# Performance work log

Hardware: AMD Instinct MI355X
Metric: run time of the kernel (lower is better)

The kernel has to match this reference:

```python
import jax, jax.numpy as jnp
import numpy as np

U, I, C, D, A, L, E = 40000, 40000, 5, 128, 64, 2, 1280000
N = U + I  # total graph nodes (users + items)
NEG_SLOPE = 0.01  # torch LeakyReLU default


def setup_inputs() -> dict:
    key = jax.random.key(0)
    ks = jax.random.split(key, 12)
    s = 0.05  # xavier-like scale
    return {
        "user_embed": jax.random.normal(ks[0], (U, C, D), jnp.float32) * s,
        "item_embed": jax.random.normal(ks[1], (I, C, D), jnp.float32) * s,
        "crit_embed": jax.random.normal(ks[2], (C, D), jnp.float32) * s,
        "gcn_weight": jax.random.normal(ks[3], (D, D), jnp.float32) * s,
        "gcn_layers": jax.random.normal(ks[4], (L, D, D), jnp.float32) * s,
        "crit_layers": jax.random.normal(ks[5], (L, D, D), jnp.float32) * s,
        "attn_p1": jax.random.normal(ks[6], (C, D, A), jnp.float32) * s,
        "attn_p2": jax.random.normal(ks[7], (C, A), jnp.float32) * s,
        "vals": jax.random.uniform(ks[8], (C, E), jnp.float32) / 16.0,
        "rows": jax.random.randint(ks[9], (C, E), 0, N, dtype=jnp.int32),
        "cols": jax.random.randint(ks[10], (C, E), 0, N, dtype=jnp.int32),
    }


def _forward(user_embed, item_embed, crit_embed, gcn_weight, gcn_layers,
             crit_layers, attn_p1, attn_p2, vals, rows, cols):
    ego = jnp.concatenate([user_embed, item_embed], axis=0)  # [N,C,D]
    bank = ego
    crit_hist = [crit_embed]  # list of [C,D], one per layer depth
    for l in range(L):
        crit_vec = crit_hist[l]  # [C,D]
        # per-criterion sparse adjacency matmul: A_c @ ego[:,c,:]
        feats = []
        for c in range(C):  # fixed small criterion count
            msg = vals[c][:, None] * jnp.take(ego[:, c, :], cols[c], axis=0)  # [E,D]
            feats.append(jax.ops.segment_sum(msg, rows[c], num_segments=N))
        gf = jnp.stack(feats, axis=1)                             # [N,C,D]
        gf = jnp.einsum('ncd,de->nce', gf, gcn_weight)            # dense GCN transform
        combined = gf * crit_vec[None, :, :]                      # criterion gating
        stacked = jax.nn.leaky_relu(
            jnp.einsum('ncd,de->nce', combined, gcn_layers[l]), NEG_SLOPE)  # [N,C,D]
        # tanh-attention aggregation, batched over the C output heads (k)
        h = jnp.tanh(jnp.einsum('ncd,kda->knca', stacked, attn_p1))  # [C,N,C,A]
        raw = jnp.einsum('knca,ka->knc', h, attn_p2)                 # [C,N,C]
        w = jax.nn.softmax(raw, axis=-1)                             # softmax over criteria
        ego = jnp.einsum('knc,ncd->nkd', w, stacked)                 # [N,C,D]
        bank = bank + ego
        crit_hist.append(crit_hist[l] @ crit_layers[l])  # [C,D]
    bank = bank / (L + 1)
    user_out = bank[:U]                                          # [U,C,D]
    item_out = jnp.concatenate(
        [bank[U:], jnp.zeros((1, C, D), bank.dtype)], axis=0)    # [I+1,C,D] dummy token
    crit_means = jnp.mean(jnp.stack(crit_hist, axis=0), axis=0)  # [C,D]
    return user_out, item_out, crit_means


def reference(user_embed, item_embed, crit_embed, gcn_weight, gcn_layers,
              crit_layers, attn_p1, attn_p2, vals, rows, cols):
    return _forward(user_embed, item_embed, crit_embed, gcn_weight, gcn_layers,
                    crit_layers, attn_p1, attn_p2, vals, rows, cols)
```

## Files before the change

### kernel.cpp

```cpp
#include <hip/hip_runtime.h>
#include <cstdint>
#include <cmath>

#define U_ 40000
#define I_ 40000
#define C_ 5
#define D_ 128
#define A_ 64
#define L_ 2
#define E_ 1280000
#define N_ (U_ + I_)
#define BINS_ (N_ * C_)
#define NEDGE_ (C_ * E_)
#define EPB_ 4096
#define NBRX_ ((NEDGE_ + EPB_ - 1) / EPB_)
#define ND1_ 1024
#define ND2_ 512

typedef __attribute__((ext_vector_type(8))) short short8;
typedef __attribute__((ext_vector_type(4))) short short4v;
typedef __attribute__((ext_vector_type(4))) float f32x4;

static __device__ __forceinline__ short f2bf(float f) {
    union { float f; uint32_t u; } x; x.f = f;
    uint32_t u = x.u;
    uint32_t r = (u + 0x7fffu + ((u >> 16) & 1u)) >> 16;
    return (short)r;
}

__global__ __launch_bounds__(256) void init_kernel(
    const float* __restrict__ user, const float* __restrict__ item,
    short* __restrict__ egob)
{
    size_t i = (size_t)blockIdx.x * 256 + threadIdx.x;
    const size_t total8 = (size_t)N_ * C_ * D_ / 8;
    const size_t user4  = (size_t)U_ * C_ * D_ / 4;
    if (i < total8) {
        size_t f4 = 2 * i;
        const float4* src = (f4 < user4) ? (const float4*)user
                                         : (const float4*)item - user4;
        float4 x0 = src[f4], x1 = src[f4 + 1];
        short8 p;
        p[0] = f2bf(x0.x); p[1] = f2bf(x0.y); p[2] = f2bf(x0.z); p[3] = f2bf(x0.w);
        p[4] = f2bf(x1.x); p[5] = f2bf(x1.y); p[6] = f2bf(x1.z); p[7] = f2bf(x1.w);
        ((short8*)egob)[i] = p;
    }
}

__global__ __launch_bounds__(128) void crit_kernel(
    const float* __restrict__ crit0, const float* __restrict__ clayers,
    float* __restrict__ crit1, float* __restrict__ crit2,
    float* __restrict__ crit_means, float* __restrict__ padrow)
{
    __shared__ float c0[C_ * D_], c1[C_ * D_], c2[C_ * D_];
    int t = threadIdx.x;
    for (int i = t; i < C_ * D_; i += 128) { c0[i] = crit0[i]; padrow[i] = 0.f; }
    __syncthreads();
    for (int c = 0; c < C_; ++c) {
        float acc = 0.f;
        for (int d = 0; d < D_; ++d) acc = fmaf(c0[c * D_ + d], clayers[d * D_ + t], acc);
        c1[c * D_ + t] = acc;
    }
    __syncthreads();
    for (int c = 0; c < C_; ++c) {
        float acc = 0.f;
        for (int d = 0; d < D_; ++d) acc = fmaf(c1[c * D_ + d], clayers[D_ * D_ + d * D_ + t], acc);
        c2[c * D_ + t] = acc;
    }
    __syncthreads();
    for (int i = t; i < C_ * D_; i += 128) {
        crit1[i] = c1[i];
        crit2[i] = c2[i];
        crit_means[i] = (c0[i] + c1[i] + c2[i]) * (1.0f / 3.0f);
    }
}

__global__ __launch_bounds__(256) void prepack_kernel(
    const float* __restrict__ W, const float* __restrict__ gl,
    short* __restrict__ Wf, short* __restrict__ Gf)
{
    int b = blockIdx.x;
    int m = b >> 3, t = b & 7;
    int q = threadIdx.x >> 6, l = threadIdx.x & 63;
    int g = l >> 4, c15 = l & 15;
    const float* src = (m == 0) ? W : gl + (size_t)(m - 1) * D_ * D_;
    short*       dst = (m == 0) ? Wf : Gf + (size_t)(m - 1) * D_ * D_;
    short8 v;
    #pragma unroll
    for (int j = 0; j < 8; ++j) {
        int k = q * 32 + g * 8 + j;
        int n = t * 16 + c15;
        v[j] = f2bf(src[k * D_ + n]);
    }
    *(short8*)(dst + (((t * 4 + q) * 64 + l) << 3)) = v;
}

__global__ __launch_bounds__(64) void prepack_p1_kernel(
    const float* __restrict__ p1, short* __restrict__ P1f)
{
    int t = blockIdx.x >> 2, q = blockIdx.x & 3;
    int lane = threadIdx.x;
    int g = lane >> 4, c15 = lane & 15;
    int k = t >> 2, a = (t & 3) * 16 + c15;
    short8 v;
    #pragma unroll
    for (int j = 0; j < 8; ++j) {
        int d = q * 32 + g * 8 + j;
        v[j] = f2bf(p1[((size_t)k * D_ + d) * A_ + a]);
    }
    *(short8*)(P1f + (((t * 4 + q) * 64 + lane) << 3)) = v;
}


__global__ __launch_bounds__(256) void p1_count_kernel(
    const int* __restrict__ rows, int* __restrict__ ghistT)
{
    __shared__ int h[ND1_];
    int b = blockIdx.x, tid = threadIdx.x;
    for (int i = tid; i < ND1_; i += 256) h[i] = 0;
    __syncthreads();
    int base = b * EPB_;
    for (int ch = 0; ch < EPB_ / 256; ++ch) {
        int eid = base + ch * 256 + tid;
        if (eid < NEDGE_) {
            int key = (eid / E_) * N_ + rows[eid];
            atomicAdd(&h[key & (ND1_ - 1)], 1);
        }
    }
    __syncthreads();
    for (int i = tid; i < ND1_; i += 256) ghistT[b * ND1_ + i] = h[i];
}

__global__ __launch_bounds__(256) void transpose_kernel(
    const int* __restrict__ src, int* __restrict__ dst, int R, int Cc)
{
    int i = blockIdx.x * 256 + threadIdx.x;
    if (i < R * Cc) { int r = i / Cc, c = i % Cc; dst[c * R + r] = src[i]; }
}

__global__ __launch_bounds__(256) void scanA_g(
    const int* __restrict__ src, int* __restrict__ dst,
    int* __restrict__ bsum, int n)
{
    __shared__ int ls[256];
    int b = blockIdx.x, t = threadIdx.x;
    int base = b * 1024 + t * 4;
    int v[4];
    #pragma unroll
    for (int i = 0; i < 4; ++i) v[i] = (base + i < n) ? src[base + i] : 0;
    int s = v[0] + v[1] + v[2] + v[3];
    ls[t] = s;
    __syncthreads();
    for (int off = 1; off < 256; off <<= 1) {
        int x = (t >= off) ? ls[t - off] : 0;
        __syncthreads();
        ls[t] += x;
        __syncthreads();
    }
    int excl = ls[t] - s;
    if (t == 255) bsum[b] = ls[255];
    #pragma unroll
    for (int i = 0; i < 4; ++i) {
        if (base + i < n) dst[base + i] = excl;
        excl += v[i];
    }
}

__global__ __launch_bounds__(256) void scanB_g(int* __restrict__ bsum, int nb)
{
    __shared__ int ls[256];
    int t = threadIdx.x;
    int v[8]; int s = 0;
    #pragma unroll
    for (int i = 0; i < 8; ++i) {
        int idx = t * 8 + i;
        v[i] = (idx < nb) ? bsum[idx] : 0;
        s += v[i];
    }
    ls[t] = s;
    __syncthreads();
    for (int off = 1; off < 256; off <<= 1) {
        int x = (t >= off) ? ls[t - off] : 0;
        __syncthreads();
        ls[t] += x;
        __syncthreads();
    }
    int excl = ls[t] - s;
    #pragma unroll
    for (int i = 0; i < 8; ++i) {
        int idx = t * 8 + i;
        if (idx < nb) bsum[idx] = excl;
        excl += v[i];
    }
}

__global__ __launch_bounds__(256) void scanC_g(
    int* __restrict__ dst, const int* __restrict__ bsum, int n)
{
    int b = blockIdx.x, t = threadIdx.x;
    int off = bsum[b];
    int base = b * 1024 + t * 4;
    #pragma unroll
    for (int i = 0; i < 4; ++i)
        if (base + i < n) dst[base + i] += off;
}

__global__ __launch_bounds__(256) void p1_place_kernel(
    const int* __restrict__ rows, const float* __restrict__ vals,
    const int* __restrict__ cols, const int* __restrict__ gbaseT,
    int* __restrict__ keyA, uint2* __restrict__ vcA)
{
    __shared__ int cur[ND1_];
    __shared__ int bst[ND1_];
    __shared__ int gb[ND1_];
    __shared__ int ts[256];
    __shared__ int sK[EPB_];
    __shared__ uint2 sV[EPB_];
    int b = blockIdx.x, tid = threadIdx.x;
    for (int i = tid; i < ND1_; i += 256) { cur[i] = 0; gb[i] = gbaseT[b * ND1_ + i]; }
    __syncthreads();
    int base = b * EPB_;
    for (int ch = 0; ch < EPB_ / 256; ++ch) {
        int eid = base + ch * 256 + tid;
        if (eid < NEDGE_) {
            int key = (eid / E_) * N_ + rows[eid];
            atomicAdd(&cur[key & (ND1_ - 1)], 1);
        }
    }
    __syncthreads();
    {
        int v[4]; int s = 0;
        #pragma unroll
        for (int i = 0; i < 4; ++i) { v[i] = cur[tid * 4 + i]; s += v[i]; }
        ts[tid] = s;
        __syncthreads();
        for (int off = 1; off < 256; off <<= 1) {
            int x = (tid >= off) ? ts[tid - off] : 0;
            __syncthreads();
            ts[tid] += x;
            __syncthreads();
        }
        int excl = ts[tid] - s;
        #pragma unroll
        for (int i = 0; i < 4; ++i) { bst[tid * 4 + i] = excl; excl += v[i]; }
        __syncthreads();
        #pragma unroll
        for (int i = 0; i < 4; ++i) cur[tid * 4 + i] = bst[tid * 4 + i];
    }
    __syncthreads();
    for (int ch = 0; ch < EPB_ / 256; ++ch) {
        int eid = base + ch * 256 + tid;
        if (eid < NEDGE_) {
            int key = (eid / E_) * N_ + rows[eid];
            int d = key & (ND1_ - 1);
            int p = atomicAdd(&cur[d], 1);
            sK[p] = key;
            union { float f; uint32_t u; } t; t.f = vals[eid];
            uint2 m; m.x = t.u; m.y = (uint32_t)cols[eid];
            sV[p] = m;
        }
    }
    __syncthreads();
    int M = NEDGE_ - base; if (M > EPB_) M = EPB_;
    for (int i = tid; i < M; i += 256) {
        int key = sK[i]; int d = key & (ND1_ - 1);
        int pos = gb[d] + (i - bst[d]);
        keyA[pos] = key; vcA[pos] = sV[i];
    }
}

__global__ __launch_bounds__(256) void p2_count_kernel(
    const int* __restrict__ keyA, int* __restrict__ ghistT)
{
    __shared__ int h[ND2_];
    int b = blockIdx.x, tid = threadIdx.x;
    for (int i = tid; i < ND2_; i += 256) h[i] = 0;
    __syncthreads();
    int base = b * EPB_;
    for (int ch = 0; ch < EPB_ / 256; ++ch) {
        int eid = base + ch * 256 + tid;
        if (eid < NEDGE_) atomicAdd(&h[keyA[eid] >> 10], 1);
    }
    __syncthreads();
    for (int i = tid; i < ND2_; i += 256) ghistT[b * ND2_ + i] = h[i];
}

__global__ __launch_bounds__(256) void p2_place_kernel(
    const int* __restrict__ keyA, const uint2* __restrict__ vcA,
    const int* __restrict__ gbaseT,
    int* __restrict__ keyB, uint2* __restrict__ vcB)
{
    __shared__ int cur[ND2_];
    __shared__ int bst[ND2_];
    __shared__ int gb[ND2_];
    __shared__ int wh[4 * ND2_];
    __shared__ int ts[256];
    __shared__ int sK[EPB_];
    __shared__ uint2 sV[EPB_];
    int b = blockIdx.x, tid = threadIdx.x;
    int lane = tid & 63, wv = tid >> 6;
    for (int i = tid; i < ND2_; i += 256) { cur[i] = 0; gb[i] = gbaseT[b * ND2_ + i]; }
    __syncthreads();
    int base = b * EPB_;
    for (int ch = 0; ch < EPB_ / 256; ++ch) {
        int eid = base + ch * 256 + tid;
        if (eid < NEDGE_) atomicAdd(&cur[keyA[eid] >> 10], 1);
    }
    __syncthreads();
    {
        int v0 = cur[tid * 2], v1 = cur[tid * 2 + 1];
        int s = v0 + v1;
        ts[tid] = s;
        __syncthreads();
        for (int off = 1; off < 256; off <<= 1) {
            int x = (tid >= off) ? ts[tid - off] : 0;
            __syncthreads();
            ts[tid] += x;
            __syncthreads();
        }
        int excl = ts[tid] - s;
        bst[tid * 2] = excl; bst[tid * 2 + 1] = excl + v0;
        __syncthreads();
        cur[tid * 2] = bst[tid * 2]; cur[tid * 2 + 1] = bst[tid * 2 + 1];
    }
    __syncthreads();
    for (int ch = 0; ch < EPB_ / 256; ++ch) {
        for (int i = tid; i < 4 * ND2_; i += 256) wh[i] = 0;
        __syncthreads();
        int eid = base + ch * 256 + tid;
        bool valid = eid < NEDGE_;
        int key = 0, d = 0; uint2 v = make_uint2(0u, 0u);
        if (valid) { key = keyA[eid]; v = vcA[eid]; d = key >> 10; }
        unsigned long long m = __ballot(valid ? 1 : 0);
        #pragma unroll
        for (int bit = 0; bit < 9; ++bit) {
            unsigned long long bb = __ballot((valid && ((d >> bit) & 1)) ? 1 : 0);
            m &= ((d >> bit) & 1) ? bb : ~bb;
        }
        unsigned long long ltm = ((unsigned long long)1 << lane) - 1;
        int rw = __popcll(m & ltm);
        int cnt = __popcll(m);
        if (valid && rw == 0) wh[wv * ND2_ + d] = cnt;
        __syncthreads();
        if (valid) {
            int off = 0;
            for (int w2 = 0; w2 < wv; ++w2) off += wh[w2 * ND2_ + d];
            int p = cur[d] + off + rw;
            sK[p] = key; sV[p] = v;
        }
        __syncthreads();
        for (int i = tid; i < ND2_; i += 256)
            cur[i] += wh[i] + wh[ND2_ + i] + wh[2 * ND2_ + i] + wh[3 * ND2_ + i];
        __syncthreads();
    }
    int M = NEDGE_ - base; if (M > EPB_) M = EPB_;
    for (int i = tid; i < M; i += 256) {
        int key = sK[i]; int d = key >> 10;
        int pos = gb[d] + (i - bst[d]);
        keyB[pos] = key; vcB[pos] = sV[i];
    }
}

__global__ __launch_bounds__(256) void boundary_kernel(
    const int* __restrict__ keyB, int* __restrict__ bin_start)
{
    int i = blockIdx.x * 256 + threadIdx.x;
    if (i >= NEDGE_) return;
    int k = keyB[i];
    if (i == 0) {
        for (int b = 0; b <= k; ++b) bin_start[b] = 0;
    } else {
        int kp = keyB[i - 1];
        for (int b = kp + 1; b <= k; ++b) bin_start[b] = i;
    }
    if (i == NEDGE_ - 1) {
        for (int b = k + 1; b <= BINS_; ++b) bin_start[b] = NEDGE_;
    }
}

__global__ __launch_bounds__(256) void gather_kernel(
    const uint4* __restrict__ eg128, const uint2* __restrict__ vc,
    const int* __restrict__ bin_start, uint4* __restrict__ gfb128)
{
    int w = (int)(((size_t)blockIdx.x * 256 + threadIdx.x) >> 6);
    int lane = threadIdx.x & 63;
    w = __builtin_amdgcn_readfirstlane(w);
    int bs = bin_start[w], be = bin_start[w + 1];
    int c = w / N_;
    int row = w - c * N_;
    int q4 = lane >> 4, l15 = lane & 15;
    float a0 = 0.f, a1 = 0.f, a2 = 0.f, a3 = 0.f;
    float a4 = 0.f, a5 = 0.f, a6 = 0.f, a7 = 0.f;

    union { uint32_t u; float f; } t;
    #define ACC8(mm, vv) \
        t.u = mm.x << 16;         a0 = fmaf(vv, t.f, a0); \
        t.u = mm.x & 0xffff0000u; a1 = fmaf(vv, t.f, a1); \
        t.u = mm.y << 16;         a2 = fmaf(vv, t.f, a2); \
        t.u = mm.y & 0xffff0000u; a3 = fmaf(vv, t.f, a3); \
        t.u = mm.z << 16;         a4 = fmaf(vv, t.f, a4); \
        t.u = mm.z & 0xffff0000u; a5 = fmaf(vv, t.f, a5); \
        t.u = mm.w << 16;         a6 = fmaf(vv, t.f, a6); \
        t.u = mm.w & 0xffff0000u; a7 = fmaf(vv, t.f, a7);

    int j = bs;
    for (; j + 16 <= be; j += 16) {
        uint2 eA = vc[j + q4];
        uint2 eB = vc[j + 4 + q4];
        uint2 eC = vc[j + 8 + q4];
        uint2 eD = vc[j + 12 + q4];
        uint4 mA = eg128[((size_t)(int)eA.y * C_ + c) * (D_ / 8) + l15];
        uint4 mB = eg128[((size_t)(int)eB.y * C_ + c) * (D_ / 8) + l15];
        uint4 mC = eg128[((size_t)(int)eC.y * C_ + c) * (D_ / 8) + l15];
        uint4 mD = eg128[((size_t)(int)eD.y * C_ + c) * (D_ / 8) + l15];
        union { uint32_t u; float f; } fv;
        fv.u = eA.x; float vA = fv.f;
        fv.u = eB.x; float vB = fv.f;
        fv.u = eC.x; float vC = fv.f;
        fv.u = eD.x; float vD = fv.f;
        ACC8(mA, vA) ACC8(mB, vB) ACC8(mC, vC) ACC8(mD, vD)
    }
    for (; j < be; j += 4) {
        int idx = j + q4;
        bool act = idx < be;
        uint2 e0 = vc[act ? idx : be - 1];
        union { uint32_t u; float f; } fv; fv.u = e0.x;
        float v0 = act ? fv.f : 0.f;
        uint4 m0 = eg128[((size_t)(int)e0.y * C_ + c) * (D_ / 8) + l15];
        ACC8(m0, v0)
    }
    #undef ACC8

    a0 += __shfl_xor(a0, 16); a1 += __shfl_xor(a1, 16);
    a2 += __shfl_xor(a2, 16); a3 += __shfl_xor(a3, 16);
    a4 += __shfl_xor(a4, 16); a5 += __shfl_xor(a5, 16);
    a6 += __shfl_xor(a6, 16); a7 += __shfl_xor(a7, 16);
    a0 += __shfl_xor(a0, 32); a1 += __shfl_xor(a1, 32);
    a2 += __shfl_xor(a2, 32); a3 += __shfl_xor(a3, 32);
    a4 += __shfl_xor(a4, 32); a5 += __shfl_xor(a5, 32);
    a6 += __shfl_xor(a6, 32); a7 += __shfl_xor(a7, 32);
    if (lane < 16) {
        uint4 o;
        o.x = (uint32_t)(uint16_t)f2bf(a0) | ((uint32_t)(uint16_t)f2bf(a1) << 16);
        o.y = (uint32_t)(uint16_t)f2bf(a2) | ((uint32_t)(uint16_t)f2bf(a3) << 16);
        o.z = (uint32_t)(uint16_t)f2bf(a4) | ((uint32_t)(uint16_t)f2bf(a5) << 16);
        o.w = (uint32_t)(uint16_t)f2bf(a6) | ((uint32_t)(uint16_t)f2bf(a7) << 16);
        gfb128[((size_t)row * C_ + c) * (D_ / 8) + l15] = o;
    }
}

__global__ __launch_bounds__(1024, 4) void rowgemm_mfma_kernel(
    const short* __restrict__ gfb, short* __restrict__ stkb,
    const short* __restrict__ Wf, const short* __restrict__ Gf,
    const float* __restrict__ critv)
{
    __shared__ short Wl[16384];
    __shared__ short Gl[16384];
    __shared__ short Zr[16][2048];

    for (int i = threadIdx.x; i < 2048; i += 1024) {
        ((short8*)Wl)[i] = ((const short8*)Wf)[i];
        ((short8*)Gl)[i] = ((const short8*)Gf)[i];
    }
    __syncthreads();

    int lane = threadIdx.x & 63, w = threadIdx.x >> 6;
    int g = lane >> 4, c15 = lane & 15;
    char* zw = (char*)&Zr[w][0];
    const int nrb = (N_ * C_ + 255) / 256;

    for (int rb = blockIdx.x; rb < nrb; rb += gridDim.x) {
        size_t r0 = (size_t)rb * 256 + (size_t)w * 16;
        if (r0 >= N_ * C_) continue;

        short8 af[4];
        #pragma unroll
        for (int q = 0; q < 4; ++q)
            af[q] = *(const short8*)(gfb + (r0 + c15) * D_ + q * 32 + g * 8);

        f32x4 acc[8];
        #pragma unroll
        for (int t = 0; t < 8; ++t) acc[t] = (f32x4){0.f, 0.f, 0.f, 0.f};
        {
            const short8* Wp = (const short8*)Wl;
            #pragma unroll
            for (int t = 0; t < 8; ++t)
                #pragma unroll
                for (int q = 0; q < 4; ++q)
                    acc[t] = __builtin_amdgcn_mfma_f32_16x16x32_bf16(
                        af[q], Wp[(t * 4 + q) * 64 + lane], acc[t], 0, 0, 0);
        }

        int rbase = (int)r0 + g * 4;
        #pragma unroll
        for (int t = 0; t < 8; ++t)
            #pragma unroll
            for (int r = 0; r < 4; ++r) {
                float cv = critv[((rbase + r) % C_) * D_ + t * 16 + c15];
                float z = acc[t][r] * cv;
                int zrow = g * 4 + r;
                int cb = 32 * t + 2 * c15;
                int off = zrow * 256 + (cb ^ ((zrow & 7) << 4));
                *(short*)(zw + off) = f2bf(z);
            }

        short8 az[4];
        #pragma unroll
        for (int q = 0; q < 4; ++q) {
            int cb0 = 64 * q + 16 * g;
            int off = c15 * 256 + (cb0 ^ ((c15 & 7) << 4));
            az[q] = *(const short8*)(zw + off);
        }

        f32x4 acc2[8];
        #pragma unroll
        for (int t = 0; t < 8; ++t) acc2[t] = (f32x4){0.f, 0.f, 0.f, 0.f};
        {
            const short8* Gp = (const short8*)Gl;
            #pragma unroll
            for (int t = 0; t < 8; ++t)
                #pragma unroll
                for (int q = 0; q < 4; ++q)
                    acc2[t] = __builtin_amdgcn_mfma_f32_16x16x32_bf16(
                        Gp[(t * 4 + q) * 64 + lane], az[q], acc2[t], 0, 0, 0);
        }

        short* srow = stkb + (r0 + c15) * D_;
        #pragma unroll
        for (int t = 0; t < 8; ++t) {
            float s0 = acc2[t][0], s1 = acc2[t][1], s2 = acc2[t][2], s3 = acc2[t][3];
            s0 = s0 > 0.f ? s0 : 0.01f * s0;
            s1 = s1 > 0.f ? s1 : 0.01f * s1;
            s2 = s2 > 0.f ? s2 : 0.01f * s2;
            s3 = s3 > 0.f ? s3 : 0.01f * s3;
            uint2 o;
            o.x = (uint32_t)(uint16_t)f2bf(s0) | ((uint32_t)(uint16_t)f2bf(s1) << 16);
            o.y = (uint32_t)(uint16_t)f2bf(s2) | ((uint32_t)(uint16_t)f2bf(s3) << 16);
            *(uint2*)(srow + t * 16 + g * 4) = o;
        }
    }
}

__global__ __launch_bounds__(256, 3) void attn_mfma_kernel(
    const short* __restrict__ stkb, const short* __restrict__ P1f,
    const float* __restrict__ p2, const float* __restrict__ user,
    const float* __restrict__ item, short* __restrict__ egob,
    float* __restrict__ bank, int last)
{
    __shared__ float rawl[80 * C_];
    __shared__ float wl[80 * C_];

    int tid = threadIdx.x;
    int lane = tid & 63, w = tid >> 6;
    int g = lane >> 4, c15 = lane & 15;
    int klo = (5 * w) >> 2;

    short8 Bf[5][4];
    float p2v[5];
    #pragma unroll
    for (int i = 0; i < 5; ++i) {
        int t = 5 * w + i;
        #pragma unroll
        for (int q = 0; q < 4; ++q)
            Bf[i][q] = ((const short8*)P1f)[(t * 4 + q) * 64 + lane];
        p2v[i] = p2[(t >> 2) * A_ + (t & 3) * 16 + c15];
    }

    float4*       bank4 = (float4*)bank;
    const float4* user4 = (const float4*)user;
    const float4* item4 = (const float4*)item;

    for (int grp = blockIdx.x; grp < N_ / 16; grp += gridDim.x) {
        size_t n0 = (size_t)grp * 16;
        for (int i = tid; i < 80 * C_; i += 256) rawl[i] = 0.f;
        __syncthreads();

        for (int rt = 0; rt < 5; ++rt) {
            short8 af[4];
            #pragma unroll
            for (int q = 0; q < 4; ++q)
                af[q] = *(const short8*)(stkb + (n0 * 5 + rt * 16 + c15) * D_ + q * 32 + g * 8);

            f32x4 acc[5];
            #pragma unroll
            for (int i = 0; i < 5; ++i) acc[i] = (f32x4){0.f, 0.f, 0.f, 0.f};
            #pragma unroll
            for (int i = 0; i < 5; ++i)
                #pragma unroll
                for (int q = 0; q < 4; ++q)
                    acc[i] = __builtin_amdgcn_mfma_f32_16x16x32_bf16(
                        af[q], Bf[i][q], acc[i], 0, 0, 0);

            float2 ps[4];
            #pragma unroll
            for (int r = 0; r < 4; ++r) ps[r] = make_float2(0.f, 0.f);
            #pragma unroll
            for (int i = 0; i < 5; ++i) {
                int t = 5 * w + i;
                bool lo = (t >> 2) == klo;
                #pragma unroll
                for (int r = 0; r < 4; ++r) {
                    float x = acc[i][r];
                    float e = __expf(2.f * x);
                    float th = 1.f - 2.f * __builtin_amdgcn_rcpf(e + 1.f);
                    float con = th * p2v[i];
                    if (lo) ps[r].x += con; else ps[r].y += con;
                }
            }
            #pragma unroll
            for (int r = 0; r < 4; ++r) {
                #pragma unroll
                for (int m = 1; m < 16; m <<= 1) {
                    ps[r].x += __shfl_xor(ps[r].x, m);
                    ps[r].y += __shfl_xor(ps[r].y, m);
                }
                if (c15 == 0) {
                    int row = rt * 16 + g * 4 + r;
                    atomicAdd(&rawl[row * C_ + klo], ps[r].x);
                    atomicAdd(&rawl[row * C_ + klo + 1], ps[r].y);
                }
            }
        }
        __syncthreads();

        if (tid < 80) {
            int nl = tid / C_, k = tid % C_;
            float rv[C_];
            #pragma unroll
            for (int c = 0; c < C_; ++c) rv[c] = rawl[(nl * C_ + c) * C_ + k];
            float m = rv[0];
            #pragma unroll
            for (int c = 1; c < C_; ++c) m = fmaxf(m, rv[c]);
            float s = 0.f;
            #pragma unroll
            for (int c = 0; c < C_; ++c) { rv[c] = __expf(rv[c] - m); s += rv[c]; }
            float inv = __builtin_amdgcn_rcpf(s);
            #pragma unroll
            for (int c = 0; c < C_; ++c) wl[tid * C_ + c] = rv[c] * inv;
        }
        __syncthreads();

        #pragma unroll
        for (int ii = 0; ii < 5; ++ii) {
            int idx = tid + 256 * ii;
            int f8 = idx & 15;
            int nl = (idx >> 4) & 15, k = idx >> 8;
            float e[8] = {0.f, 0.f, 0.f, 0.f, 0.f, 0.f, 0.f, 0.f};
            #pragma unroll
            for (int c = 0; c < C_; ++c) {
                float wv = wl[(nl * C_ + k) * C_ + c];
                uint4 sv = ((const uint4*)(stkb + ((n0 + nl) * C_ + c) * D_))[f8];
                union { uint32_t u; float f; } t;
                t.u = sv.x << 16;         e[0] = fmaf(wv, t.f, e[0]);
                t.u = sv.x & 0xffff0000u; e[1] = fmaf(wv, t.f, e[1]);
                t.u = sv.y << 16;         e[2] = fmaf(wv, t.f, e[2]);
                t.u = sv.y & 0xffff0000u; e[3] = fmaf(wv, t.f, e[3]);
                t.u = sv.z << 16;         e[4] = fmaf(wv, t.f, e[4]);
                t.u = sv.z & 0xffff0000u; e[5] = fmaf(wv, t.f, e[5]);
                t.u = sv.w << 16;         e[6] = fmaf(wv, t.f, e[6]);
                t.u = sv.w & 0xffff0000u; e[7] = fmaf(wv, t.f, e[7]);
            }
            size_t n = n0 + nl;
            size_t go = ((n * 5 + k) * 16 + f8) * 8;
            if (!last) {
                short8 pk;
                #pragma unroll
                for (int x = 0; x < 8; ++x) pk[x] = f2bf(e[x]);
                *(short8*)(egob + go) = pk;
            } else {
                uint4 e0 = *(const uint4*)(egob + go);
                size_t bo = (n * 5 + k) * 32 + f8 * 2;
                float4 b0 = (n < U_) ? user4[((size_t)n * C_ + k) * 32 + f8 * 2]
                                     : item4[((size_t)(n - U_) * C_ + k) * 32 + f8 * 2];
                float4 b1 = (n < U_) ? user4[((size_t)n * C_ + k) * 32 + f8 * 2 + 1]
                                     : item4[((size_t)(n - U_) * C_ + k) * 32 + f8 * 2 + 1];
                union { uint32_t u; float f; } t;
                t.u = e0.x << 16;         b0.x += t.f + e[0];
                t.u = e0.x & 0xffff0000u; b0.y += t.f + e[1];
                t.u = e0.y << 16;         b0.z += t.f + e[2];
                t.u = e0.y & 0xffff0000u; b0.w += t.f + e[3];
                t.u = e0.z << 16;         b1.x += t.f + e[4];
                t.u = e0.z & 0xffff0000u; b1.y += t.f + e[5];
                t.u = e0.w << 16;         b1.z += t.f + e[6];
                t.u = e0.w & 0xffff0000u; b1.w += t.f + e[7];
                b0.x *= (1.f / 3.f); b0.y *= (1.f / 3.f);
                b0.z *= (1.f / 3.f); b0.w *= (1.f / 3.f);
                b1.x *= (1.f / 3.f); b1.y *= (1.f / 3.f);
                b1.z *= (1.f / 3.f); b1.w *= (1.f / 3.f);
                bank4[bo] = b0;
                bank4[bo + 1] = b1;
            }
        }
    }
}

extern "C" void kernel_launch(void* const* d_in, const int* in_sizes, int n_in,
                              void* d_out, int out_size, void* d_ws, size_t ws_size,
                              hipStream_t stream) {
    const float* user  = (const float*)d_in[0];
    const float* item  = (const float*)d_in[1];
    const float* crit0 = (const float*)d_in[2];
    const float* W     = (const float*)d_in[3];
    const float* gl    = (const float*)d_in[4];
    const float* cl    = (const float*)d_in[5];
    const float* p1    = (const float*)d_in[6];
    const float* p2    = (const float*)d_in[7];
    const float* vals  = (const float*)d_in[8];
    const int*   rows  = (const int*)d_in[9];
    const int*   cols  = (const int*)d_in[10];

    float* out  = (float*)d_out;
    float* bank = out;
    float* padrow = out + (size_t)N_ * C_ * D_;
    float* crit_means = out + (size_t)(N_ + 1) * C_ * D_;

    const size_t NCD = (size_t)N_ * C_ * D_;
    short* egob  = (short*)d_ws;
    short* gfb   = egob + NCD;
    short* stkb  = gfb + NCD;
    float* crit1 = (float*)(stkb + NCD);
    float* crit2 = crit1 + C_ * D_;
    short* Wf    = (short*)(crit2 + C_ * D_);
    short* Gf    = Wf + (size_t)D_ * D_;
    short* P1f   = Gf + 2 * (size_t)D_ * D_;
    int* bin_start = (int*)(P1f + (size_t)D_ * C_ * A_);
    int* keyB      = bin_start + BINS_ + 2;
    uint2* vcB     = (uint2*)(keyB + NEDGE_);
    int* ghist     = (int*)(vcB + NEDGE_);
    int* ghistT    = ghist + (size_t)ND1_ * NBRX_;
    int* bsum      = ghistT + (size_t)ND1_ * NBRX_;
    uint2* vcA = (uint2*)stkb;
    int*  keyA = (int*)((char*)stkb + (size_t)NEDGE_ * 8);

    init_kernel<<<(int)((NCD / 8 + 255) / 256), 256, 0, stream>>>(user, item, egob);
    crit_kernel<<<1, 128, 0, stream>>>(crit0, cl, crit1, crit2, crit_means, padrow);
    prepack_kernel<<<24, 256, 0, stream>>>(W, gl, Wf, Gf);
    prepack_p1_kernel<<<80, 64, 0, stream>>>(p1, P1f);

    const int n1 = ND1_ * NBRX_, n2 = ND2_ * NBRX_;
    p1_count_kernel<<<NBRX_, 256, 0, stream>>>(rows, ghistT);
    transpose_kernel<<<(n1 + 255) / 256, 256, 0, stream>>>(ghistT, ghist, NBRX_, ND1_);
    scanA_g<<<(n1 + 1023) / 1024, 256, 0, stream>>>(ghist, ghist, bsum, n1);
    scanB_g<<<1, 256, 0, stream>>>(bsum, (n1 + 1023) / 1024);
    scanC_g<<<(n1 + 1023) / 1024, 256, 0, stream>>>(ghist, bsum, n1);
    transpose_kernel<<<(n1 + 255) / 256, 256, 0, stream>>>(ghist, ghistT, ND1_, NBRX_);
    p1_place_kernel<<<NBRX_, 256, 0, stream>>>(rows, vals, cols, ghistT, keyA, vcA);

    p2_count_kernel<<<NBRX_, 256, 0, stream>>>(keyA, ghistT);
    transpose_kernel<<<(n2 + 255) / 256, 256, 0, stream>>>(ghistT, ghist, NBRX_, ND2_);
    scanA_g<<<(n2 + 1023) / 1024, 256, 0, stream>>>(ghist, ghist, bsum, n2);
    scanB_g<<<1, 256, 0, stream>>>(bsum, (n2 + 1023) / 1024);
    scanC_g<<<(n2 + 1023) / 1024, 256, 0, stream>>>(ghist, bsum, n2);
    transpose_kernel<<<(n2 + 255) / 256, 256, 0, stream>>>(ghist, ghistT, ND2_, NBRX_);
    p2_place_kernel<<<NBRX_, 256, 0, stream>>>(keyA, vcA, ghistT, keyB, vcB);

    boundary_kernel<<<(NEDGE_ + 255) / 256, 256, 0, stream>>>(keyB, bin_start);

    for (int l = 0; l < L_; ++l) {
        gather_kernel<<<BINS_ / 4, 256, 0, stream>>>(
            (const uint4*)egob, vcB, bin_start, (uint4*)gfb);
        rowgemm_mfma_kernel<<<256, 1024, 0, stream>>>(
            gfb, stkb, Wf, Gf + (size_t)l * D_ * D_, l == 0 ? crit0 : crit1);
        attn_mfma_kernel<<<768, 256, 0, stream>>>(
            stkb, P1f, p2, user, item, egob, bank, l == L_ - 1 ? 1 : 0);
    }
}
```

Measured before the change: 1.335 ms.

## Reuse saved per-block histograms in place kernels and shuffle-broadcast edge metadata in gather

The count kernels now also save each block's per-bucket histogram to a separate buffer. The place kernels read those counts instead of re-reading the keys and redoing shared-memory atomics, which removes a full pass over the edge data and some barriers. The gather kernel now loads up to 64 edge (value, column) pairs cooperatively, one per lane, and broadcasts them with shuffles, instead of having each 4-lane group reload them from global memory. The trade-off is an extra histogram buffer placed after bsum, which relies on the workspace being large enough, plus extra shuffle instructions in the gather inner loop.

```diff
diff --git a/kernel.cpp b/kernel.cpp
--- a/kernel.cpp
+++ b/kernel.cpp
@@ -113,7 +113,8 @@
 
 
 __global__ __launch_bounds__(256) void p1_count_kernel(
-    const int* __restrict__ rows, int* __restrict__ ghistT)
+    const int* __restrict__ rows, int* __restrict__ ghistT,
+    int* __restrict__ gcntT)
 {
     __shared__ int h[ND1_];
     int b = blockIdx.x, tid = threadIdx.x;
@@ -128,7 +129,10 @@
         }
     }
     __syncthreads();
-    for (int i = tid; i < ND1_; i += 256) ghistT[b * ND1_ + i] = h[i];
+    for (int i = tid; i < ND1_; i += 256) {
+        ghistT[b * ND1_ + i] = h[i];
+        gcntT[b * ND1_ + i] = h[i];
+    }
 }
 
 __global__ __launch_bounds__(256) void transpose_kernel(
@@ -208,6 +212,7 @@
 __global__ __launch_bounds__(256) void p1_place_kernel(
     const int* __restrict__ rows, const float* __restrict__ vals,
     const int* __restrict__ cols, const int* __restrict__ gbaseT,
+    const int* __restrict__ gcntT,
     int* __restrict__ keyA, uint2* __restrict__ vcA)
 {
     __shared__ int cur[ND1_];
@@ -217,21 +222,11 @@
     __shared__ int sK[EPB_];
     __shared__ uint2 sV[EPB_];
     int b = blockIdx.x, tid = threadIdx.x;
-    for (int i = tid; i < ND1_; i += 256) { cur[i] = 0; gb[i] = gbaseT[b * ND1_ + i]; }
-    __syncthreads();
-    int base = b * EPB_;
-    for (int ch = 0; ch < EPB_ / 256; ++ch) {
-        int eid = base + ch * 256 + tid;
-        if (eid < NEDGE_) {
-            int key = (eid / E_) * N_ + rows[eid];
-            atomicAdd(&cur[key & (ND1_ - 1)], 1);
-        }
-    }
-    __syncthreads();
+    for (int i = tid; i < ND1_; i += 256) gb[i] = gbaseT[b * ND1_ + i];
     {
         int v[4]; int s = 0;
         #pragma unroll
-        for (int i = 0; i < 4; ++i) { v[i] = cur[tid * 4 + i]; s += v[i]; }
+        for (int i = 0; i < 4; ++i) { v[i] = gcntT[b * ND1_ + tid * 4 + i]; s += v[i]; }
         ts[tid] = s;
         __syncthreads();
         for (int off = 1; off < 256; off <<= 1) {
@@ -242,12 +237,10 @@
         }
         int excl = ts[tid] - s;
         #pragma unroll
-        for (int i = 0; i < 4; ++i) { bst[tid * 4 + i] = excl; excl += v[i]; }
-        __syncthreads();
-        #pragma unroll
-        for (int i = 0; i < 4; ++i) cur[tid * 4 + i] = bst[tid * 4 + i];
-    }
-    __syncthreads();
+        for (int i = 0; i < 4; ++i) { bst[tid * 4 + i] = excl; cur[tid * 4 + i] = excl; excl += v[i]; }
+    }
+    __syncthreads();
+    int base = b * EPB_;
     for (int ch = 0; ch < EPB_ / 256; ++ch) {
         int eid = base + ch * 256 + tid;
         if (eid < NEDGE_) {
@@ -270,7 +263,8 @@
 }
 
 __global__ __launch_bounds__(256) void p2_count_kernel(
-    const int* __restrict__ keyA, int* __restrict__ ghistT)
+    const int* __restrict__ keyA, int* __restrict__ ghistT,
+    int* __restrict__ gcntT)
 {
     __shared__ int h[ND2_];
     int b = blockIdx.x, tid = threadIdx.x;
@@ -282,12 +276,15 @@
         if (eid < NEDGE_) atomicAdd(&h[keyA[eid] >> 10], 1);
     }
     __syncthreads();
-    for (int i = tid; i < ND2_; i += 256) ghistT[b * ND2_ + i] = h[i];
+    for (int i = tid; i < ND2_; i += 256) {
+        ghistT[b * ND2_ + i] = h[i];
+        gcntT[b * ND2_ + i] = h[i];
+    }
 }
 
 __global__ __launch_bounds__(256) void p2_place_kernel(
     const int* __restrict__ keyA, const uint2* __restrict__ vcA,
-    const int* __restrict__ gbaseT,
+    const int* __restrict__ gbaseT, const int* __restrict__ gcntT,
     int* __restrict__ keyB, uint2* __restrict__ vcB)
 {
     __shared__ int cur[ND2_];
@@ -299,16 +296,10 @@
     __shared__ uint2 sV[EPB_];
     int b = blockIdx.x, tid = threadIdx.x;
     int lane = tid & 63, wv = tid >> 6;
-    for (int i = tid; i < ND2_; i += 256) { cur[i] = 0; gb[i] = gbaseT[b * ND2_ + i]; }
-    __syncthreads();
-    int base = b * EPB_;
-    for (int ch = 0; ch < EPB_ / 256; ++ch) {
-        int eid = base + ch * 256 + tid;
-        if (eid < NEDGE_) atomicAdd(&cur[keyA[eid] >> 10], 1);
-    }
-    __syncthreads();
+    for (int i = tid; i < ND2_; i += 256) gb[i] = gbaseT[b * ND2_ + i];
+    for (int i = tid; i < 4 * ND2_; i += 256) wh[i] = 0;
     {
-        int v0 = cur[tid * 2], v1 = cur[tid * 2 + 1];
+        int v0 = gcntT[b * ND2_ + tid * 2], v1 = gcntT[b * ND2_ + tid * 2 + 1];
         int s = v0 + v1;
         ts[tid] = s;
         __syncthreads();
@@ -320,13 +311,11 @@
         }
         int excl = ts[tid] - s;
         bst[tid * 2] = excl; bst[tid * 2 + 1] = excl + v0;
-        __syncthreads();
-        cur[tid * 2] = bst[tid * 2]; cur[tid * 2 + 1] = bst[tid * 2 + 1];
-    }
-    __syncthreads();
+        cur[tid * 2] = excl; cur[tid * 2 + 1] = excl + v0;
+    }
+    __syncthreads();
+    int base = b * EPB_;
     for (int ch = 0; ch < EPB_ / 256; ++ch) {
-        for (int i = tid; i < 4 * ND2_; i += 256) wh[i] = 0;
-        __syncthreads();
         int eid = base + ch * 256 + tid;
         bool valid = eid < NEDGE_;
         int key = 0, d = 0; uint2 v = make_uint2(0u, 0u);
@@ -349,8 +338,10 @@
             sK[p] = key; sV[p] = v;
         }
         __syncthreads();
-        for (int i = tid; i < ND2_; i += 256)
+        for (int i = tid; i < ND2_; i += 256) {
             cur[i] += wh[i] + wh[ND2_ + i] + wh[2 * ND2_ + i] + wh[3 * ND2_ + i];
+            wh[i] = 0; wh[ND2_ + i] = 0; wh[2 * ND2_ + i] = 0; wh[3 * ND2_ + i] = 0;
+        }
         __syncthreads();
     }
     int M = NEDGE_ - base; if (M > EPB_) M = EPB_;
@@ -392,45 +383,45 @@
     float a0 = 0.f, a1 = 0.f, a2 = 0.f, a3 = 0.f;
     float a4 = 0.f, a5 = 0.f, a6 = 0.f, a7 = 0.f;
 
-    union { uint32_t u; float f; } t;
-    #define ACC8(mm, vv) \
-        t.u = mm.x << 16;         a0 = fmaf(vv, t.f, a0); \
-        t.u = mm.x & 0xffff0000u; a1 = fmaf(vv, t.f, a1); \
-        t.u = mm.y << 16;         a2 = fmaf(vv, t.f, a2); \
-        t.u = mm.y & 0xffff0000u; a3 = fmaf(vv, t.f, a3); \
-        t.u = mm.z << 16;         a4 = fmaf(vv, t.f, a4); \
-        t.u = mm.z & 0xffff0000u; a5 = fmaf(vv, t.f, a5); \
-        t.u = mm.w << 16;         a6 = fmaf(vv, t.f, a6); \
-        t.u = mm.w & 0xffff0000u; a7 = fmaf(vv, t.f, a7);
-
-    int j = bs;
-    for (; j + 16 <= be; j += 16) {
-        uint2 eA = vc[j + q4];
-        uint2 eB = vc[j + 4 + q4];
-        uint2 eC = vc[j + 8 + q4];
-        uint2 eD = vc[j + 12 + q4];
-        uint4 mA = eg128[((size_t)(int)eA.y * C_ + c) * (D_ / 8) + l15];
-        uint4 mB = eg128[((size_t)(int)eB.y * C_ + c) * (D_ / 8) + l15];
-        uint4 mC = eg128[((size_t)(int)eC.y * C_ + c) * (D_ / 8) + l15];
-        uint4 mD = eg128[((size_t)(int)eD.y * C_ + c) * (D_ / 8) + l15];
-        union { uint32_t u; float f; } fv;
-        fv.u = eA.x; float vA = fv.f;
-        fv.u = eB.x; float vB = fv.f;
-        fv.u = eC.x; float vC = fv.f;
-        fv.u = eD.x; float vD = fv.f;
-        ACC8(mA, vA) ACC8(mB, vB) ACC8(mC, vC) ACC8(mD, vD)
-    }
-    for (; j < be; j += 4) {
-        int idx = j + q4;
-        bool act = idx < be;
-        uint2 e0 = vc[act ? idx : be - 1];
-        union { uint32_t u; float f; } fv; fv.u = e0.x;
-        float v0 = act ? fv.f : 0.f;
-        uint4 m0 = eg128[((size_t)(int)e0.y * C_ + c) * (D_ / 8) + l15];
-        ACC8(m0, v0)
-    }
-    #undef ACC8
-
+    for (int base = bs; base < be; base += 64) {
+        int cnt = be - base; if (cnt > 64) cnt = 64;
+        float v = 0.f; int s = 0;
+        if (lane < cnt) {
+            uint2 m = vc[base + lane];
+            union { uint32_t u; float f; } t; t.u = m.x;
+            v = t.f; s = (int)m.y;
+        }
+        int j = 0;
+        for (; j + 16 <= cnt; j += 16) {
+            float v0 = __shfl(v, j + q4),      v1 = __shfl(v, j + 4 + q4);
+            float v2 = __shfl(v, j + 8 + q4),  v3 = __shfl(v, j + 12 + q4);
+            int   s0 = __shfl(s, j + q4),      s1 = __shfl(s, j + 4 + q4);
+            int   s2 = __shfl(s, j + 8 + q4),  s3 = __shfl(s, j + 12 + q4);
+            uint4 m0 = eg128[((size_t)s0 * C_ + c) * (D_ / 8) + l15];
+            uint4 m1 = eg128[((size_t)s1 * C_ + c) * (D_ / 8) + l15];
+            uint4 m2 = eg128[((size_t)s2 * C_ + c) * (D_ / 8) + l15];
+            uint4 m3 = eg128[((size_t)s3 * C_ + c) * (D_ / 8) + l15];
+            union { uint32_t u; float f; } t;
+            #define ACC8(mm, vv) \
+                t.u = mm.x << 16;         a0 = fmaf(vv, t.f, a0); \
+                t.u = mm.x & 0xffff0000u; a1 = fmaf(vv, t.f, a1); \
+                t.u = mm.y << 16;         a2 = fmaf(vv, t.f, a2); \
+                t.u = mm.y & 0xffff0000u; a3 = fmaf(vv, t.f, a3); \
+                t.u = mm.z << 16;         a4 = fmaf(vv, t.f, a4); \
+                t.u = mm.z & 0xffff0000u; a5 = fmaf(vv, t.f, a5); \
+                t.u = mm.w << 16;         a6 = fmaf(vv, t.f, a6); \
+                t.u = mm.w & 0xffff0000u; a7 = fmaf(vv, t.f, a7);
+            ACC8(m0, v0) ACC8(m1, v1) ACC8(m2, v2) ACC8(m3, v3)
+        }
+        for (; j < cnt; j += 4) {
+            float v0 = __shfl(v, j + q4);
+            int   s0 = __shfl(s, j + q4);
+            uint4 m0 = eg128[((size_t)s0 * C_ + c) * (D_ / 8) + l15];
+            union { uint32_t u; float f; } t;
+            ACC8(m0, v0)
+            #undef ACC8
+        }
+    }
     a0 += __shfl_xor(a0, 16); a1 += __shfl_xor(a1, 16);
     a2 += __shfl_xor(a2, 16); a3 += __shfl_xor(a3, 16);
     a4 += __shfl_xor(a4, 16); a5 += __shfl_xor(a5, 16);
@@ -729,6 +720,7 @@
     int* ghist     = (int*)(vcB + NEDGE_);
     int* ghistT    = ghist + (size_t)ND1_ * NBRX_;
     int* bsum      = ghistT + (size_t)ND1_ * NBRX_;
+    int* gcntT     = bsum + 2048;
     uint2* vcA = (uint2*)stkb;
     int*  keyA = (int*)((char*)stkb + (size_t)NEDGE_ * 8);
 
@@ -738,21 +730,21 @@
     prepack_p1_kernel<<<80, 64, 0, stream>>>(p1, P1f);
 
     const int n1 = ND1_ * NBRX_, n2 = ND2_ * NBRX_;
-    p1_count_kernel<<<NBRX_, 256, 0, stream>>>(rows, ghistT);
+    p1_count_kernel<<<NBRX_, 256, 0, stream>>>(rows, ghistT, gcntT);
     transpose_kernel<<<(n1 + 255) / 256, 256, 0, stream>>>(ghistT, ghist, NBRX_, ND1_);
     scanA_g<<<(n1 + 1023) / 1024, 256, 0, stream>>>(ghist, ghist, bsum, n1);
     scanB_g<<<1, 256, 0, stream>>>(bsum, (n1 + 1023) / 1024);
     scanC_g<<<(n1 + 1023) / 1024, 256, 0, stream>>>(ghist, bsum, n1);
     transpose_kernel<<<(n1 + 255) / 256, 256, 0, stream>>>(ghist, ghistT, ND1_, NBRX_);
-    p1_place_kernel<<<NBRX_, 256, 0, stream>>>(rows, vals, cols, ghistT, keyA, vcA);
-
-    p2_count_kernel<<<NBRX_, 256, 0, stream>>>(keyA, ghistT);
+    p1_place_kernel<<<NBRX_, 256, 0, stream>>>(rows, vals, cols, ghistT, gcntT, keyA, vcA);
+
+    p2_count_kernel<<<NBRX_, 256, 0, stream>>>(keyA, ghistT, gcntT);
     transpose_kernel<<<(n2 + 255) / 256, 256, 0, stream>>>(ghistT, ghist, NBRX_, ND2_);
     scanA_g<<<(n2 + 1023) / 1024, 256, 0, stream>>>(ghist, ghist, bsum, n2);
     scanB_g<<<1, 256, 0, stream>>>(bsum, (n2 + 1023) / 1024);
     scanC_g<<<(n2 + 1023) / 1024, 256, 0, stream>>>(ghist, bsum, n2);
     transpose_kernel<<<(n2 + 255) / 256, 256, 0, stream>>>(ghist, ghistT, ND2_, NBRX_);
-    p2_place_kernel<<<NBRX_, 256, 0, stream>>>(keyA, vcA, ghistT, keyB, vcB);
+    p2_place_kernel<<<NBRX_, 256, 0, stream>>>(keyA, vcA, ghistT, gcntT, keyB, vcB);
 
     boundary_kernel<<<(NEDGE_ + 255) / 256, 256, 0, stream>>>(keyB, bin_start);
 
```

Result: faster. 1.264 ms (-5.3%).
